# Kernel tuning notes

Hardware: AMD Instinct MI355X
Metric: run time of the kernel (lower is better)

## Reference

```python
import jax, jax.numpy as jnp
import numpy as np

N_NODES = 4096
HID = 64
N_STEP = 10
_OFFSETS = np.array([1, 2, 5, 11, 23, 47, 97, 193])  # circulant graph -> degree 16


def setup_inputs() -> dict:
    rng = np.random.default_rng(0)
    N = N_NODES
    i = np.repeat(np.arange(N), len(_OFFSETS))
    j = (i + np.tile(_OFFSETS, N)) % N
    vals = rng.normal(0.0, 0.5, i.shape).astype(np.float32)
    J = np.zeros((N, N), np.float32)
    J[i, j] = vals
    J[j, i] = vals  # symmetric coupling matrix
    row, col = np.nonzero(J)                      # E directed edges, row-major sorted
    key_fwd = row.astype(np.int64) * N + col
    rev = np.searchsorted(key_fwd, col.astype(np.int64) * N + row)  # reverse-edge index
    ru, cu = np.nonzero(np.triu(J))               # Eu upper-triangular edges
    u2e = np.searchsorted(key_fwd, ru.astype(np.int64) * N + cu)    # upper -> full edge index
    bias = rng.normal(0.0, 0.5, N).astype(np.float32)
    p = lambda *s: jnp.asarray(rng.normal(0.0, 0.1, s).astype(np.float32))
    return {
        'J': jnp.asarray(J), 'bias': jnp.asarray(bias),
        'gat_W': p(4, HID), 'gat_a': p(2 * HID, 1),
        'ci_W1': p(4, HID), 'ci_b1': jnp.zeros((HID,), jnp.float32),
        'ci_W2': p(HID, HID), 'ci_b2': jnp.zeros((HID,), jnp.float32),
        'ci_W3': p(HID, 1), 'ci_b3': jnp.zeros((1,), jnp.float32),
        'row': jnp.asarray(row.astype(np.int32)), 'col': jnp.asarray(col.astype(np.int32)),
        'rev': jnp.asarray(rev.astype(np.int32)),
        'ru': jnp.asarray(ru.astype(np.int32)), 'cu': jnp.asarray(cu.astype(np.int32)),
        'u2e': jnp.asarray(u2e.astype(np.int32)),
        'N_step': N_STEP, 'MPNNtype': 0,
    }


def reference(J, bias, gat_W, gat_a, ci_W1, ci_b1, ci_W2, ci_b2, ci_W3, ci_b3,
              row, col, rev, ru, cu, u2e, N_step, MPNNtype):
    N = J.shape[0]
    adj = (jnp.abs(J) > 0).astype(J.dtype)
    # node features: [-b, b, degree, row-sum of J]
    feat = jnp.stack([-bias, bias, adj.sum(1), J.sum(1)], axis=1)  # [N,4]
    # GAT scores: e[i,j] = leakyrelu([Wh_i || Wh_j] @ a) = leakyrelu(Wh_i@a1 + Wh_j@a2)
    Wh = feat @ gat_W                                  # [N,H]
    f1 = Wh @ gat_a[:HID, 0]
    f2 = Wh @ gat_a[HID:, 0]
    e = jax.nn.leaky_relu(f1[:, None] + f2[None, :], 0.2)
    att = jnp.where(adj > 0, jnp.exp(e), 0.0)
    Cij_matrix = 0.5 * (att + att.T)                   # [N,N]
    Cij_e = Cij_matrix[row, col]                       # [E]
    # Ci readout MLP
    h = jax.nn.relu(feat @ ci_W1 + ci_b1)
    h = jax.nn.relu(h @ ci_W2 + ci_b2)
    Ci = h @ ci_W3 + ci_b3                             # [N,1]
    dom = Ci + Cij_matrix.sum(1, keepdims=True)
    dom = jnp.sign(dom) * jnp.maximum(jnp.abs(dom), 0.1)  # clamp |.| >= 0.1
    bias_scale = bias / dom[:, 0]
    bx_scale = jnp.stack([-bias_scale, bias_scale], axis=1)  # [N,2]
    Jv = J[row, col]
    Jxy_scale = jnp.stack([jnp.stack([Jv, -Jv], -1),
                           jnp.stack([-Jv, Jv], -1)], axis=1) / Cij_e[:, None, None]  # [E,2,2]

    def node_update(em):
        # node_messages[j,:] = sum over edges (i->j) of em[e,:]
        nm = jax.ops.segment_sum(em, col, num_segments=N) / dom   # [N,2]
        lnZ = jnp.log(jnp.sum(jnp.exp(bx_scale + nm), axis=1, keepdims=True))
        return bx_scale + nm - lnZ, lnZ

    em0 = jnp.zeros((row.shape[0], 2), J.dtype)  # log of all-ones messages
    hidden0, lnZ0 = node_update(em0)

    def bp_step(carry, _):
        em, hidden, lnZ = carry
        ln_pj = hidden[row][:, :, None]     # [E,2,1]
        ln_zj = lnZ[row][:, :, None]        # [E,1,1]
        ln_mu_ij = em[rev][:, :, None]      # message on reverse edge, [E,2,1]
        M = jnp.exp(Jxy_scale + ln_pj + ln_zj - ln_mu_ij)          # [E,2,2]
        M = M / jnp.sum(jnp.max(M, axis=1), axis=1)[:, None, None]
        em_new = jnp.log(jnp.max(M ** Cij_e[:, None, None], axis=1))  # [E,2]
        hidden_new, lnZ_new = node_update(em_new)
        return (em_new, hidden_new, lnZ_new), None

    (em, hidden, lnZ), _ = jax.lax.scan(bp_step, (em0, hidden0, lnZ0), None, length=N_step)

    readout = jnp.exp(hidden)                           # [N,2]
    Js = J[ru, cu] / Cij_matrix[ru, cu]                 # [Eu]
    Jxy_u = jnp.exp(jnp.stack([jnp.stack([Js, -Js], -1),
                               jnp.stack([-Js, Js], -1)], axis=1))  # [Eu,2,2]
    temp_i = readout[cu] / jnp.exp(em[u2e])             # [Eu,2]
    temp_j = readout[ru] / jnp.exp(em[rev[u2e]])        # [Eu,2]
    pw = Jxy_u * temp_i[:, None, :] * temp_j[:, :, None]
    pw = pw / jnp.sum(pw, axis=(1, 2), keepdims=True)
    readout_pairwise = pw.reshape(-1, 4)                # [Eu,4]
    Cij_u = Cij_matrix[ru, cu]
    node_H = -jnp.sum(readout * jnp.log(readout + 1e-16), axis=1)
    edge_H = -jnp.sum(readout_pairwise * jnp.log(readout_pairwise + 1e-16), axis=1)
    node_entropy = Ci[:, 0] @ jax.lax.stop_gradient(node_H)
    edge_entropy = Cij_u @ jax.lax.stop_gradient(edge_H)
    return (readout, readout_pairwise, node_entropy + edge_entropy,
            node_entropy, edge_entropy, Ci[:, 0], Cij_u, dom)
```

## Files before the change

kernel.cpp:

```cpp
#include <hip/hip_runtime.h>
#include <cstddef>

#define TB    512
#define NB    128
#define NSTEP 10
#define SENTV 0xFFFFFFFFFFFFFFFFULL

__device__ __forceinline__ float lse2(float a, float b) {
    return fmaxf(a, b) + __logf(1.0f + __expf(-fabsf(a - b)));
}

__device__ __forceinline__ void stA(float2* p, float2 v) {
    union { float2 f; unsigned long long u; } x; x.f = v;
    __hip_atomic_store((unsigned long long*)p, x.u,
                       __ATOMIC_RELAXED, __HIP_MEMORY_SCOPE_AGENT);
}
__device__ __forceinline__ float2 pollLd(const float2* p) {
    union { float2 f; unsigned long long u; } x;
    x.u = __hip_atomic_load((const unsigned long long*)p,
                            __ATOMIC_RELAXED, __HIP_MEMORY_SCOPE_AGENT);
    while (x.u == SENTV) {
        __builtin_amdgcn_s_sleep(1);
        x.u = __hip_atomic_load((const unsigned long long*)p,
                                __ATOMIC_RELAXED, __HIP_MEMORY_SCOPE_AGENT);
    }
    return x.f;
}

struct KParams {
    const float *J, *bias, *gat_W, *gat_a, *W1, *b1, *W2, *b2, *W3, *b3;
    const int *col, *rev, *ru, *cu, *u2e;
    int N, Eu;
    float2 *fA, *jsC, *em, *uS;
    float  *ci_out, *dom_out, *ent;
    float2* ro_out;
    float4* rp_out;
    float*  cij_out;
};

__global__ __launch_bounds__(TB) void k_fused(KParams p) {
    __shared__ float sW2[64 * 64];
    __shared__ float sh1[TB / 16][65];
    __shared__ float red[TB / 64];

    const int tidb = threadIdx.x;
    const int g = blockIdx.x * TB + tidb;
    const int i = g >> 4, t = g & 15;
    const int lane = tidb & 63;
    const int N = p.N;

    for (int k = tidb; k < 64 * 64; k += TB) sW2[k] = p.W2[k];
    if (g < 3) {
        __hip_atomic_store((int*)&p.ent[g], 0,
                           __ATOMIC_RELAXED, __HIP_MEMORY_SCOPE_AGENT);
    }

    const int j  = p.col[g];
    const float Jv = p.J[(size_t)i * (size_t)N + (size_t)j];

    float rs = Jv;
    rs += __shfl_xor(rs, 1); rs += __shfl_xor(rs, 2);
    rs += __shfl_xor(rs, 4); rs += __shfl_xor(rs, 8);

    const float bi = p.bias[i];

    float s8 = 0.0f;
    if (lane < 8) {
        int k = lane & 3;
        const float* a = p.gat_a + ((lane < 4) ? 0 : 64);
        for (int h = 0; h < 64; ++h) s8 += p.gat_W[k * 64 + h] * a[h];
    }
    const float w10 = __shfl(s8, 0), w11 = __shfl(s8, 1), w12 = __shfl(s8, 2), w13 = __shfl(s8, 3);
    const float w20 = __shfl(s8, 4), w21 = __shfl(s8, 5), w22 = __shfl(s8, 6), w23 = __shfl(s8, 7);
    const float fd = 16.0f;
    const float f1i = -bi * w10 + bi * w11 + fd * w12 + rs * w13;
    const float f2i = -bi * w20 + bi * w21 + fd * w22 + rs * w23;
    if (t == 0) stA(&p.fA[i], make_float2(f1i, f2i));

    const int nib = tidb >> 4;
    __syncthreads();
    #pragma unroll
    for (int m = 0; m < 4; ++m) {
        int h = t + 16 * m;
        float a = -bi * p.W1[h] + bi * p.W1[64 + h] + fd * p.W1[128 + h]
                + rs * p.W1[192 + h] + p.b1[h];
        sh1[nib][h] = fmaxf(a, 0.0f);
    }
    __syncthreads();
    float civ = 0.0f;
    #pragma unroll
    for (int m = 0; m < 4; ++m) {
        int o = t + 16 * m;
        float acc = p.b2[o];
        for (int h = 0; h < 64; ++h) acc += sh1[nib][h] * sW2[h * 64 + o];
        civ += fmaxf(acc, 0.0f) * p.W3[o];
    }
    civ += __shfl_xor(civ, 1); civ += __shfl_xor(civ, 2);
    civ += __shfl_xor(civ, 4); civ += __shfl_xor(civ, 8);
    const float ci = civ + p.b3[0];

    const float2 fj = pollLd(&p.fA[j]);
    float x1 = f1i + fj.y; x1 = (x1 > 0.0f) ? x1 : 0.2f * x1;
    float x2 = fj.x + f2i; x2 = (x2 > 0.0f) ? x2 : 0.2f * x2;
    const float C  = 0.5f * (__expf(x1) + __expf(x2));
    const float js = Jv / C;
    stA(&p.jsC[g], make_float2(js, C));

    float sc = C;
    sc += __shfl_xor(sc, 1); sc += __shfl_xor(sc, 2);
    sc += __shfl_xor(sc, 4); sc += __shfl_xor(sc, 8);
    const float s  = ci + sc;
    const float cl = fmaxf(fabsf(s), 0.1f);
    const float d  = (s > 0.0f) ? cl : ((s < 0.0f) ? -cl : 0.0f);
    const float rd = 1.0f / d;
    const float bs = bi * rd;
    if (t == 0) {
        p.ci_out[i] = ci;
        p.dom_out[i] = d;
        stA(&p.uS[i], make_float2(-bs, bs));
    }

    int eE = 0, eR = 0, eC = 0, eEr = 0;
    if (g < p.Eu) {
        eE = p.u2e[g]; eR = p.ru[g]; eC = p.cu[g];
        eEr = p.rev[eE];
    }

    float in0 = 0.0f, in1 = 0.0f;
    float out0 = 0.0f, out1 = 0.0f;
    float ui0 = -bs, ui1 = bs;
    for (int st = 0; st < NSTEP; ++st) {
        const float2 uj = pollLd(&p.uS[(size_t)st * N + j]);
        const float a0 = uj.x - out0, a1 = uj.y - out1;
        const float t0 = fmaxf( js + a0, -js + a1);
        const float t1 = fmaxf(-js + a0,  js + a1);
        const float ls = lse2(t0, t1);
        const float ni0 = C * (t0 - ls), ni1 = C * (t1 - ls);
        const float b0 = ui0 - in0, b1 = ui1 - in1;
        const float q0 = fmaxf( js + b0, -js + b1);
        const float q1 = fmaxf(-js + b0,  js + b1);
        const float qs = lse2(q0, q1);
        out0 = C * (q0 - qs); out1 = C * (q1 - qs);
        in0 = ni0; in1 = ni1;

        float nm0 = in0, nm1 = in1;
        nm0 += __shfl_xor(nm0, 1); nm1 += __shfl_xor(nm1, 1);
        nm0 += __shfl_xor(nm0, 2); nm1 += __shfl_xor(nm1, 2);
        nm0 += __shfl_xor(nm0, 4); nm1 += __shfl_xor(nm1, 4);
        nm0 += __shfl_xor(nm0, 8); nm1 += __shfl_xor(nm1, 8);
        ui0 = -bs + nm0 * rd; ui1 = bs + nm1 * rd;
        if (t == 0) stA(&p.uS[(size_t)(st + 1) * N + i], make_float2(ui0, ui1));
        if (st == NSTEP - 1) stA(&p.em[g], make_float2(in0, in1));
    }

    float nodeC = 0.0f;
    if (t == 0) {
        const float lz = lse2(ui0, ui1);
        const float r0 = __expf(ui0 - lz), r1 = __expf(ui1 - lz);
        p.ro_out[i] = make_float2(r0, r1);
        const float H = -(r0 * __logf(r0 + 1e-16f) + r1 * __logf(r1 + 1e-16f));
        nodeC = ci * H;
    }
    for (int off = 32; off > 0; off >>= 1) nodeC += __shfl_down(nodeC, off);
    {
        const int wv = tidb >> 6;
        if (lane == 0) red[wv] = nodeC;
        __syncthreads();
        if (tidb == 0) {
            float sn = 0.0f;
            #pragma unroll
            for (int w = 0; w < TB / 64; ++w) sn += red[w];
            atomicAdd(&p.ent[0], sn);
            atomicAdd(&p.ent[1], sn);
        }
        __syncthreads();
    }

    const float2* uF = p.uS + (size_t)NSTEP * N;
    float edgeC = 0.0f;
    if (g < p.Eu) {
        const float2 jc = pollLd(&p.jsC[eE]);
        const float jse = jc.x, Ce = jc.y;
        const float2 uc = pollLd(&uF[eC]), ur = pollLd(&uF[eR]);
        const float2 eme = pollLd(&p.em[eEr]);
        const float2 emr = pollLd(&p.em[eE]);
        const float lc = lse2(uc.x, uc.y);
        const float lr = lse2(ur.x, ur.y);
        const float ti0 = (uc.x - lc) - eme.x, ti1 = (uc.y - lc) - eme.y;
        const float tj0 = (ur.x - lr) - emr.x, tj1 = (ur.y - lr) - emr.y;
        const float L00 =  jse + ti0 + tj0;
        const float L01 = -jse + ti1 + tj0;
        const float L10 = -jse + ti0 + tj1;
        const float L11 =  jse + ti1 + tj1;
        const float mL = fmaxf(fmaxf(L00, L01), fmaxf(L10, L11));
        float p00 = __expf(L00 - mL), p01 = __expf(L01 - mL);
        float p10 = __expf(L10 - mL), p11 = __expf(L11 - mL);
        const float inv = 1.0f / (p00 + p01 + p10 + p11);
        p00 *= inv; p01 *= inv; p10 *= inv; p11 *= inv;
        p.rp_out[g] = make_float4(p00, p01, p10, p11);
        p.cij_out[g] = Ce;
        const float H = -(p00 * __logf(p00 + 1e-16f) + p01 * __logf(p01 + 1e-16f)
                        + p10 * __logf(p10 + 1e-16f) + p11 * __logf(p11 + 1e-16f));
        edgeC = Ce * H;
    }
    for (int off = 32; off > 0; off >>= 1) edgeC += __shfl_down(edgeC, off);
    const int wv = tidb >> 6;
    if (lane == 0) red[wv] = edgeC;
    __syncthreads();
    if (tidb == 0) {
        float se = 0.0f;
        #pragma unroll
        for (int w = 0; w < TB / 64; ++w) se += red[w];
        atomicAdd(&p.ent[0], se);
        atomicAdd(&p.ent[2], se);
    }
}

extern "C" void kernel_launch(void* const* d_in, const int* in_sizes, int n_in,
                              void* d_out, int out_size, void* d_ws, size_t ws_size,
                              hipStream_t stream) {
    const int N  = in_sizes[1];
    const int E  = in_sizes[10];
    const int Eu = in_sizes[13];

    float* out = (float*)d_out;
    size_t OFF_RP  = 2 * (size_t)N;
    size_t OFF_ENT = OFF_RP + 4 * (size_t)Eu;

    char* w = (char*)d_ws;
    auto carve = [&](size_t bytes) {
        void* q = (void*)w;
        w += (bytes + 255) & ~(size_t)255;
        return q;
    };

    KParams p;
    p.J     = (const float*)d_in[0];
    p.bias  = (const float*)d_in[1];
    p.gat_W = (const float*)d_in[2];
    p.gat_a = (const float*)d_in[3];
    p.W1    = (const float*)d_in[4];
    p.b1    = (const float*)d_in[5];
    p.W2    = (const float*)d_in[6];
    p.b2    = (const float*)d_in[7];
    p.W3    = (const float*)d_in[8];
    p.b3    = (const float*)d_in[9];
    p.col   = (const int*)d_in[11];
    p.rev   = (const int*)d_in[12];
    p.ru    = (const int*)d_in[13];
    p.cu    = (const int*)d_in[14];
    p.u2e   = (const int*)d_in[15];
    p.N = N; p.Eu = Eu;

    const size_t szFA = (size_t)N * 8;
    const size_t szJC = (size_t)E * 8;
    const size_t szEM = (size_t)E * 8;
    const size_t szUS = (size_t)(NSTEP + 1) * N * 8;
    p.fA  = (float2*)carve(szFA);
    p.jsC = (float2*)carve(szJC);
    p.em  = (float2*)carve(szEM);
    p.uS  = (float2*)carve(szUS);

    p.ro_out  = (float2*)out;
    p.rp_out  = (float4*)(out + OFF_RP);
    p.ent     = out + OFF_ENT;
    p.ci_out  = p.ent + 3;
    p.cij_out = p.ci_out + N;
    p.dom_out = p.cij_out + Eu;

    hipMemsetAsync(p.fA, 0xFF, szFA + szJC + szEM + szUS, stream);
    k_fused<<<dim3(NB), dim3(TB), 0, stream>>>(p);
}
```

Measured before the change: 157.2 us.

## Vectorize MLP with transposed float4 W2 and defer out-message compute past store

W2 is stored transposed in shared memory as padded float4 rows, and each thread's hidden row is held in registers, so the 64x64 MLP reads shared memory with vector loads. One __syncthreads is dropped, since the W2 staging is still covered by the barrier after the sh1 writes. In the BP loop, the outgoing-message computation is moved after the reduction and the store of this step's node state, so the store reaches other blocks earlier and the critical chain between polling blocks gets shorter. This adds register pressure from the 16 float4 registers.

```diff
diff --git a/kernel.cpp b/kernel.cpp
--- a/kernel.cpp
+++ b/kernel.cpp
@@ -39,9 +39,9 @@
 };
 
 __global__ __launch_bounds__(TB) void k_fused(KParams p) {
-    __shared__ float sW2[64 * 64];
-    __shared__ float sh1[TB / 16][65];
-    __shared__ float red[TB / 64];
+    __shared__ float4 sW2T[64 * 17];
+    __shared__ float  sh1[TB / 16][68];
+    __shared__ float  red[TB / 64];
 
     const int tidb = threadIdx.x;
     const int g = blockIdx.x * TB + tidb;
@@ -49,7 +49,12 @@
     const int lane = tidb & 63;
     const int N = p.N;
 
-    for (int k = tidb; k < 64 * 64; k += TB) sW2[k] = p.W2[k];
+    for (int idx = tidb; idx < 64 * 16; idx += TB) {
+        const int o = idx >> 4, hh = idx & 15;
+        sW2T[o * 17 + hh] = make_float4(
+            p.W2[(4 * hh + 0) * 64 + o], p.W2[(4 * hh + 1) * 64 + o],
+            p.W2[(4 * hh + 2) * 64 + o], p.W2[(4 * hh + 3) * 64 + o]);
+    }
     if (g < 3) {
         __hip_atomic_store((int*)&p.ent[g], 0,
                            __ATOMIC_RELAXED, __HIP_MEMORY_SCOPE_AGENT);
@@ -78,7 +83,6 @@
     if (t == 0) stA(&p.fA[i], make_float2(f1i, f2i));
 
     const int nib = tidb >> 4;
-    __syncthreads();
     #pragma unroll
     for (int m = 0; m < 4; ++m) {
         int h = t + 16 * m;
@@ -87,12 +91,24 @@
         sh1[nib][h] = fmaxf(a, 0.0f);
     }
     __syncthreads();
+    float4 hv[16];
+    {
+        const float4* hrow = (const float4*)&sh1[nib][0];
+        #pragma unroll
+        for (int hh = 0; hh < 16; ++hh) hv[hh] = hrow[hh];
+    }
     float civ = 0.0f;
     #pragma unroll
     for (int m = 0; m < 4; ++m) {
-        int o = t + 16 * m;
+        const int o = t + 16 * m;
+        const float4* wrow = &sW2T[o * 17];
         float acc = p.b2[o];
-        for (int h = 0; h < 64; ++h) acc += sh1[nib][h] * sW2[h * 64 + o];
+        #pragma unroll
+        for (int hh = 0; hh < 16; ++hh) {
+            const float4 wv = wrow[hh];
+            acc += hv[hh].x * wv.x + hv[hh].y * wv.y
+                 + hv[hh].z * wv.z + hv[hh].w * wv.w;
+        }
         civ += fmaxf(acc, 0.0f) * p.W3[o];
     }
     civ += __shfl_xor(civ, 1); civ += __shfl_xor(civ, 2);
@@ -136,11 +152,8 @@
         const float t1 = fmaxf(-js + a0,  js + a1);
         const float ls = lse2(t0, t1);
         const float ni0 = C * (t0 - ls), ni1 = C * (t1 - ls);
-        const float b0 = ui0 - in0, b1 = ui1 - in1;
-        const float q0 = fmaxf( js + b0, -js + b1);
-        const float q1 = fmaxf(-js + b0,  js + b1);
-        const float qs = lse2(q0, q1);
-        out0 = C * (q0 - qs); out1 = C * (q1 - qs);
+        const float pu0 = ui0, pu1 = ui1;
+        const float pi0 = in0, pi1 = in1;
         in0 = ni0; in1 = ni1;
 
         float nm0 = in0, nm1 = in1;
@@ -151,6 +164,12 @@
         ui0 = -bs + nm0 * rd; ui1 = bs + nm1 * rd;
         if (t == 0) stA(&p.uS[(size_t)(st + 1) * N + i], make_float2(ui0, ui1));
         if (st == NSTEP - 1) stA(&p.em[g], make_float2(in0, in1));
+
+        const float b0 = pu0 - pi0, b1 = pu1 - pi1;
+        const float q0 = fmaxf( js + b0, -js + b1);
+        const float q1 = fmaxf(-js + b0,  js + b1);
+        const float qs = lse2(q0, q1);
+        out0 = C * (q0 - qs); out1 = C * (q1 - qs);
     }
 
     float nodeC = 0.0f;
```

New measurement: 157.3 us. No clear change (+0.1%).
